# Performance work log

Measured on AMD Instinct MI355X. Metric: run time of the kernel, lower is better.

## Reference

```python
import jax, jax.numpy as jnp
import numpy as np

DIM = 256
HEADS = 8
WS = 8      # window size
SS = 4      # shift size
EPS = 1e-5
HEAD_DIM = DIM // HEADS
SCALE = HEAD_DIM ** (-0.5)
N = WS * WS

# relative position index, replicating tf.meshgrid default 'xy' indexing
_ch = np.arange(WS)
_coords = np.stack(np.meshgrid(_ch, _ch, indexing='xy'))          # [2, WS, WS]
_flat = _coords.reshape(2, -1)                                     # [2, N]
_rel = _flat[:, :, None] - _flat[:, None, :]                       # [2, N, N]
_rel = _rel.transpose(1, 2, 0) + np.array([WS - 1, WS - 1])
_rel = _rel * np.array([2 * WS - 1, 1])
RPI = jnp.asarray(_rel.sum(-1).reshape(-1))                        # [N*N] int


def _calc_mask(H, W):
    # faithful to source: mask is -100 where window region ids are EQUAL, 0 otherwise
    img = np.zeros((H, W))
    slices = (slice(0, -WS), slice(-WS, -SS), slice(-SS, None))
    cnt = 0
    for hs in slices:
        for ws_ in slices:
            img[hs, ws_] = cnt
            cnt += 1
    mw = img.reshape(H // WS, WS, W // WS, WS).transpose(0, 2, 1, 3).reshape(-1, N)
    diff = mw[:, None, :] - mw[:, :, None]
    mask = np.where(diff == 0, -100.0, 0.0).astype(np.float32)     # [nW, N, N]
    return jnp.asarray(mask)


def _layernorm(x, g, b):
    m = jnp.mean(x, axis=-1, keepdims=True)
    v = jnp.mean(jnp.square(x - m), axis=-1, keepdims=True)
    return (x - m) * jax.lax.rsqrt(v + EPS) * g + b


def setup_inputs() -> dict:
    key = jax.random.key(0)
    ks = jax.random.split(key, 8)
    B, L, C = 16, 64 * 64, DIM
    s = 0.02
    return {
        'x': jax.random.normal(ks[0], (B, L, C), jnp.float32),
        'norm1_g': jnp.ones((C,), jnp.float32),
        'norm1_b': jnp.zeros((C,), jnp.float32),
        'qkv_w': jax.random.normal(ks[1], (C, 3 * C), jnp.float32) * s,
        'qkv_b': jnp.zeros((3 * C,), jnp.float32),
        'rpb_table': jax.random.normal(ks[2], ((2 * WS - 1) ** 2, HEADS), jnp.float32) * s,
        'proj_w': jax.random.normal(ks[3], (C, C), jnp.float32) * s,
        'proj_b': jnp.zeros((C,), jnp.float32),
        'norm2_g': jnp.ones((C,), jnp.float32),
        'norm2_b': jnp.zeros((C,), jnp.float32),
        'fc1_w': jax.random.normal(ks[4], (C, 4 * C), jnp.float32) * s,
        'fc1_b': jnp.zeros((4 * C,), jnp.float32),
        'fc2_w': jax.random.normal(ks[5], (4 * C, C), jnp.float32) * s,
        'fc2_b': jnp.zeros((C,), jnp.float32),
        'h': 64,
        'w': 64,
    }


def reference(x, norm1_g, norm1_b, qkv_w, qkv_b, rpb_table, proj_w, proj_b,
              norm2_g, norm2_b, fc1_w, fc1_b, fc2_w, fc2_b, h, w):
    B, L, C = x.shape
    nH, nW = h // WS, w // WS
    nWin = nH * nW
    shortcut = x

    xn = _layernorm(x, norm1_g, norm1_b).reshape(B, h, w, C)
    xn = jnp.roll(xn, shift=(-SS, -SS), axis=(1, 2))                 # cyclic shift
    # window partition -> [B*nWin, N, C]
    xw = xn.reshape(B, nH, WS, nW, WS, C).transpose(0, 1, 3, 2, 4, 5).reshape(B * nWin, N, C)

    qkv = (xw @ qkv_w + qkv_b).reshape(B * nWin, N, 3, HEADS, HEAD_DIM)
    qkv = qkv.transpose(2, 0, 3, 1, 4)                               # [3, B*nWin, H, N, d]
    q, k, v = qkv[0] * SCALE, qkv[1], qkv[2]

    attn = jnp.einsum('bhnd,bhmd->bhnm', q, k)                       # [B*nWin, H, N, N]
    bias = rpb_table[RPI].reshape(N, N, HEADS).transpose(2, 0, 1)    # [H, N, N]
    attn = attn + bias[None]

    mask = _calc_mask(h, w)                                          # [nWin, N, N]
    attn = attn.reshape(B, nWin, HEADS, N, N) + mask[None, :, None]
    attn = jax.nn.softmax(attn, axis=-1).reshape(B * nWin, HEADS, N, N)

    out = jnp.einsum('bhnm,bhmd->bhnd', attn, v)                     # [B*nWin, H, N, d]
    out = out.transpose(0, 2, 1, 3).reshape(B * nWin, N, C)
    out = out @ proj_w + proj_b

    # window reverse + reverse shift
    out = out.reshape(B, nH, nW, WS, WS, C).transpose(0, 1, 3, 2, 4, 5).reshape(B, h, w, C)
    out = jnp.roll(out, shift=(SS, SS), axis=(1, 2)).reshape(B, h * w, C)

    y = shortcut + out
    m = _layernorm(y, norm2_g, norm2_b)
    m = jax.nn.gelu(m @ fc1_w + fc1_b, approximate=False) @ fc2_w + fc2_b
    # faithful to source: final residual reuses the ORIGINAL shortcut, not y
    return shortcut + m
```

## Files before the change

kernel.cpp:

```cpp
#include <hip/hip_runtime.h>
#include <math.h>

typedef __bf16 bf16;
typedef __bf16 bf16x4 __attribute__((ext_vector_type(4)));
typedef __bf16 bf16x8 __attribute__((ext_vector_type(8)));
typedef float f32x4 __attribute__((ext_vector_type(4)));

#define AS1 __attribute__((address_space(1)))
#define AS3 __attribute__((address_space(3)))

__device__ __forceinline__ void gload_lds16(const bf16* g, bf16* l) {
    __builtin_amdgcn_global_load_lds((const AS1 void*)g, (AS3 void*)l, 16, 0, 0);
}

__device__ __forceinline__ float gelu_fast(float v) {
    const float u = 1.5957691216057308f * (v + 0.044715f * v * v * v);
    return v / (1.0f + __expf(-u));
}

__global__ __launch_bounds__(256)
void wprep_all(const float* __restrict__ qkv_w, const float* __restrict__ proj_w,
               const float* __restrict__ fc1_w, const float* __restrict__ fc2_w,
               bf16* __restrict__ qkv_wt, bf16* __restrict__ proj_wt,
               bf16* __restrict__ fc1_wt, bf16* __restrict__ fc2_wt)
{
    int idx = blockIdx.x * 256 + threadIdx.x;
    const float* src; bf16* dst; int K, N;
    if (idx < 196608)            { src = qkv_w;  dst = qkv_wt;  K = 256;  N = 768; }
    else if (idx < 262144)       { idx -= 196608; src = proj_w; dst = proj_wt; K = 256;  N = 256; }
    else if (idx < 524288)       { idx -= 262144; src = fc1_w;  dst = fc1_wt;  K = 256;  N = 1024; }
    else                         { idx -= 524288; src = fc2_w;  dst = fc2_wt;  K = 1024; N = 256; }
    const int k = idx / N, n = idx % N;
    dst[(long)n * K + k] = (bf16)src[idx];
}

__global__ __launch_bounds__(256)
void ln1_window(const float* __restrict__ x, const float* __restrict__ g,
                const float* __restrict__ be, bf16* __restrict__ xw)
{
    const int t = threadIdx.x;
    const int lane = t & 63;
    const int w = t >> 6;
    const long tok = (long)blockIdx.x * 4 + w;
    const float4 v = ((const float4*)(x + tok * 256))[lane];
    float sum = v.x + v.y + v.z + v.w;
    float sq  = v.x * v.x + v.y * v.y + v.z * v.z + v.w * v.w;
#pragma unroll
    for (int m = 32; m >= 1; m >>= 1) {
        sum += __shfl_xor(sum, m, 64);
        sq  += __shfl_xor(sq,  m, 64);
    }
    const float mean = sum * (1.0f / 256.0f);
    const float var  = sq * (1.0f / 256.0f) - mean * mean;
    const float rstd = rsqrtf(var + 1e-5f);
    const float4 gv = ((const float4*)g)[lane];
    const float4 bv = ((const float4*)be)[lane];
    bf16x4 ov;
    ov[0] = (bf16)((v.x - mean) * rstd * gv.x + bv.x);
    ov[1] = (bf16)((v.y - mean) * rstd * gv.y + bv.y);
    ov[2] = (bf16)((v.z - mean) * rstd * gv.z + bv.z);
    ov[3] = (bf16)((v.w - mean) * rstd * gv.w + bv.w);
    const int b = (int)(tok >> 12);
    const int l = (int)(tok & 4095);
    const int i = l >> 6, j = l & 63;
    const int ip = (i + 60) & 63, jp = (j + 60) & 63;
    const int winl = ((ip >> 3) << 3) + (jp >> 3);
    const int n = ((ip & 7) << 3) + (jp & 7);
    const long drow = ((long)b * 64 + winl) * 64 + n;
    *(bf16x4*)(xw + drow * 256 + lane * 4) = ov;
}

__global__ __launch_bounds__(256)
void ln2_kernel(const float* __restrict__ x, const bf16* __restrict__ pj,
                const float* __restrict__ g, const float* __restrict__ be,
                bf16* __restrict__ xn2)
{
    const int t = threadIdx.x;
    const int lane = t & 63;
    const int w = t >> 6;
    const long tok = (long)blockIdx.x * 4 + w;
    const float4 xv = ((const float4*)(x + tok * 256))[lane];
    const bf16x4 pv = *(const bf16x4*)(pj + tok * 256 + lane * 4);
    float y0 = xv.x + (float)pv[0];
    float y1 = xv.y + (float)pv[1];
    float y2 = xv.z + (float)pv[2];
    float y3 = xv.w + (float)pv[3];
    float sum = y0 + y1 + y2 + y3;
    float sq  = y0 * y0 + y1 * y1 + y2 * y2 + y3 * y3;
#pragma unroll
    for (int m = 32; m >= 1; m >>= 1) {
        sum += __shfl_xor(sum, m, 64);
        sq  += __shfl_xor(sq,  m, 64);
    }
    const float mean = sum * (1.0f / 256.0f);
    const float var  = sq * (1.0f / 256.0f) - mean * mean;
    const float rstd = rsqrtf(var + 1e-5f);
    const float4 gv = ((const float4*)g)[lane];
    const float4 bv = ((const float4*)be)[lane];
    bf16x4 ov;
    ov[0] = (bf16)((y0 - mean) * rstd * gv.x + bv.x);
    ov[1] = (bf16)((y1 - mean) * rstd * gv.y + bv.y);
    ov[2] = (bf16)((y2 - mean) * rstd * gv.z + bv.z);
    ov[3] = (bf16)((y3 - mean) * rstd * gv.w + bv.w);
    *(bf16x4*)(xn2 + tok * 256 + lane * 4) = ov;
}

template<int EPI>
__global__ __launch_bounds__(512, 2)
void gemm_w(const bf16* __restrict__ A, const bf16* __restrict__ Bt,
            const float* __restrict__ bias, void* __restrict__ outp,
            int N, int K, const float* __restrict__ xres, int gx, int nb)
{
    extern __shared__ bf16 lds[];
    bf16* sA = lds;
    bf16* sB = lds + 3 * 8192;
    const int t = threadIdx.x;
    const int l = t & 63;
    const int w = t >> 6;
    const int wr = w >> 1, wc = w & 1;
    const int q = nb >> 3;
    const int id = ((int)blockIdx.x & 7) * q + ((int)blockIdx.x >> 3);
    const long m0 = (long)(id / gx) * 256;
    const long n0 = (long)(id % gx) * 128;

    long asrc[2]; int adst[2];
#pragma unroll
    for (int j = 0; j < 2; j++) {
        const int idx = j * 512 + t;
        const int p = idx >> 3, s = idx & 7;
        const int sl = s ^ (p & 7);
        const int row = 2 * p + (sl >> 2);
        const int ce = (sl & 3) * 8;
        asrc[j] = (m0 + row) * (long)K + ce;
        adst[j] = idx * 8;
    }
    long bsrc; int bdst;
    {
        const int idx = t;
        const int p = idx >> 3, s = idx & 7;
        const int sl = s ^ (p & 7);
        const int row = 2 * p + (sl >> 2);
        const int ce = (sl & 3) * 8;
        bsrc = (n0 + row) * (long)K + ce;
        bdst = idx * 8;
    }

    f32x4 acc[4][4];
#pragma unroll
    for (int i = 0; i < 4; i++)
#pragma unroll
        for (int j = 0; j < 4; j++) acc[i][j] = (f32x4){0.f, 0.f, 0.f, 0.f};

    const int KT = K >> 5;
    const int c = l >> 4;
    const int ra = wr * 64 + (l & 15);
    const int rb = wc * 64 + (l & 15);

#define STAGE(bufi, ko)                                                        \
    do {                                                                       \
        gload_lds16(A + asrc[0] + (ko), &sA[(bufi) * 8192 + adst[0]]);         \
        gload_lds16(A + asrc[1] + (ko), &sA[(bufi) * 8192 + adst[1]]);         \
        gload_lds16(Bt + bsrc + (ko), &sB[(bufi) * 4096 + bdst]);              \
    } while (0)

#define COMPUTE(bufi)                                                          \
    do {                                                                       \
        bf16x8 av[4], bv[4];                                                   \
        _Pragma("unroll")                                                      \
        for (int ni = 0; ni < 4; ni++) {                                       \
            const int row = rb + ni * 16;                                      \
            const int p = row >> 1;                                            \
            const int s = (((row & 1) << 2) + c) ^ (p & 7);                    \
            bv[ni] = *(const bf16x8*)&sB[(bufi) * 4096 + (p * 8 + s) * 8];     \
        }                                                                      \
        _Pragma("unroll")                                                      \
        for (int mi = 0; mi < 4; mi++) {                                       \
            const int row = ra + mi * 16;                                      \
            const int p = row >> 1;                                            \
            const int s = (((row & 1) << 2) + c) ^ (p & 7);                    \
            av[mi] = *(const bf16x8*)&sA[(bufi) * 8192 + (p * 8 + s) * 8];     \
        }                                                                      \
        _Pragma("unroll")                                                      \
        for (int mi = 0; mi < 4; mi++)                                         \
            _Pragma("unroll")                                                  \
            for (int ni = 0; ni < 4; ni++)                                     \
                acc[mi][ni] = __builtin_amdgcn_mfma_f32_16x16x32_bf16(         \
                    bv[ni], av[mi], acc[mi][ni], 0, 0, 0);                     \
    } while (0)

    STAGE(0, 0);
    STAGE(1, 32);

    int buf = 0;
    for (int kt = 0; kt < KT - 1; ++kt) {
        asm volatile("s_waitcnt vmcnt(3)" ::: "memory");
        __builtin_amdgcn_s_barrier();
        __builtin_amdgcn_sched_barrier(0);
        if (kt + 2 < KT) {
            const int nbuf = (buf + 2 >= 3) ? buf - 1 : buf + 2;
            STAGE(nbuf, (long)(kt + 2) * 32);
        }
        COMPUTE(buf);
        buf = (buf + 1 == 3) ? 0 : buf + 1;
    }
    asm volatile("s_waitcnt vmcnt(0)" ::: "memory");
    __builtin_amdgcn_s_barrier();
    __builtin_amdgcn_sched_barrier(0);
    COMPUTE(buf);
#undef STAGE
#undef COMPUTE

#pragma unroll
    for (int mi = 0; mi < 4; mi++)
#pragma unroll
        for (int ni = 0; ni < 4; ni++) {
            const long row = m0 + wr * 64 + mi * 16 + (l & 15);
            const int col = (int)(n0 + wc * 64 + ni * 16 + (l >> 4) * 4);
            const float4 bz = *(const float4*)&bias[col];
            float v0 = acc[mi][ni][0] + bz.x;
            float v1 = acc[mi][ni][1] + bz.y;
            float v2 = acc[mi][ni][2] + bz.z;
            float v3 = acc[mi][ni][3] + bz.w;
            if constexpr (EPI == 2) {
                v0 = gelu_fast(v0); v1 = gelu_fast(v1);
                v2 = gelu_fast(v2); v3 = gelu_fast(v3);
            }
            if constexpr (EPI == 3) {
                const float4 xr = *(const float4*)&xres[row * N + col];
                float4 ov = {v0 + xr.x, v1 + xr.y, v2 + xr.z, v3 + xr.w};
                *(float4*)&((float*)outp)[row * N + col] = ov;
            } else {
                bf16x4 ov;
                ov[0] = (bf16)v0; ov[1] = (bf16)v1; ov[2] = (bf16)v2; ov[3] = (bf16)v3;
                if constexpr (EPI == 1) {
                    const int gwin = (int)(row >> 6);
                    const int n = (int)(row & 63);
                    const int bb = gwin >> 6, wi = gwin & 63;
                    const int ipp = ((wi >> 3) << 3) + (n >> 3);
                    const int jpp = ((wi & 7) << 3) + (n & 7);
                    const int ii = (ipp + 4) & 63, jj = (jpp + 4) & 63;
                    const long tok = ((long)bb << 12) + (ii << 6) + jj;
                    *(bf16x4*)&((bf16*)outp)[tok * 256 + col] = ov;
                } else {
                    *(bf16x4*)&((bf16*)outp)[row * N + col] = ov;
                }
            }
        }
    (void)xres;
}

__global__ __launch_bounds__(256, 2)
void attn_kernel(const bf16* __restrict__ qkv, const float* __restrict__ rpb,
                 bf16* __restrict__ out)
{
    __shared__ bf16 P_lds[4][64 * 64];
    const int t = threadIdx.x;
    const int lane = t & 63;
    const int w = t >> 6;
    const int win = blockIdx.x;
    const int wi = win & 63;
    const int lr = lane & 15;
    const int lg = lane >> 4;
    const int lk = lg * 8;
    const long base = (long)win * 64 * 768;
    const float scale = 0.17677669529663687f;
    const int whb = (wi >> 3) << 3;
    const int wwb = (wi & 7) << 3;
    const f32x4 z4 = {0.f, 0.f, 0.f, 0.f};

    for (int hh = 0; hh < 2; hh++) {
        const int head = w + hh * 4;
        const bf16* qp = qkv + base + head * 32;
        const bf16* kp = qkv + base + 256 + head * 32;
        const bf16* vp = qkv + base + 512 + head * 32;

        bf16x8 aq[4], bk[4];
#pragma unroll
        for (int mi = 0; mi < 4; mi++)
            aq[mi] = *(const bf16x8*)(qp + (mi * 16 + lr) * 768 + lk);
#pragma unroll
        for (int ni = 0; ni < 4; ni++)
            bk[ni] = *(const bf16x8*)(kp + (ni * 16 + lr) * 768 + lk);

        f32x4 s[4][4];
#pragma unroll
        for (int i = 0; i < 4; i++)
#pragma unroll
            for (int j = 0; j < 4; j++) s[i][j] = z4;
#pragma unroll
        for (int mi = 0; mi < 4; mi++)
#pragma unroll
            for (int ni = 0; ni < 4; ni++)
                s[mi][ni] = __builtin_amdgcn_mfma_f32_16x16x32_bf16(aq[mi], bk[ni], s[mi][ni], 0, 0, 0);

#pragma unroll
        for (int mi = 0; mi < 4; mi++)
#pragma unroll
            for (int r = 0; r < 4; r++) {
                const int n = mi * 16 + lg * 4 + r;
                const int gi = whb + (n >> 3);
                const int gj = wwb + (n & 7);
                const int idn = (gi < 56 ? 0 : (gi < 60 ? 1 : 2)) * 3 + (gj < 56 ? 0 : (gj < 60 ? 1 : 2));
                float vals[4];
                float rowmax = -3.0e38f;
#pragma unroll
                for (int ni = 0; ni < 4; ni++) {
                    const int m = ni * 16 + lr;
                    const int gi2 = whb + (m >> 3);
                    const int gj2 = wwb + (m & 7);
                    const int idm = (gi2 < 56 ? 0 : (gi2 < 60 ? 1 : 2)) * 3 + (gj2 < 56 ? 0 : (gj2 < 60 ? 1 : 2));
                    const int dj = (n & 7) - (m & 7);
                    const int di = (n >> 3) - (m >> 3);
                    float sv = s[mi][ni][r] * scale + rpb[((dj + 7) * 15 + (di + 7)) * 8 + head];
                    if (idn == idm) sv -= 100.0f;
                    vals[ni] = sv;
                    rowmax = fmaxf(rowmax, sv);
                }
#pragma unroll
                for (int msk = 8; msk >= 1; msk >>= 1)
                    rowmax = fmaxf(rowmax, __shfl_xor(rowmax, msk, 64));
                float rsum = 0.f;
#pragma unroll
                for (int ni = 0; ni < 4; ni++) {
                    const float p = __expf(vals[ni] - rowmax);
                    vals[ni] = p;
                    rsum += p;
                }
#pragma unroll
                for (int msk = 8; msk >= 1; msk >>= 1)
                    rsum += __shfl_xor(rsum, msk, 64);
                const float inv = 1.0f / rsum;
#pragma unroll
                for (int ni = 0; ni < 4; ni++)
                    P_lds[w][n * 64 + ni * 16 + lr] = (bf16)(vals[ni] * inv);
            }

        f32x4 o[4][2];
#pragma unroll
        for (int i = 0; i < 4; i++)
#pragma unroll
            for (int j = 0; j < 2; j++) o[i][j] = z4;
#pragma unroll
        for (int kk = 0; kk < 2; kk++) {
            bf16x8 bv[2];
#pragma unroll
            for (int ni = 0; ni < 2; ni++)
#pragma unroll
                for (int i = 0; i < 8; i++)
                    bv[ni][i] = vp[(kk * 32 + lk + i) * 768 + ni * 16 + lr];
#pragma unroll
            for (int mi = 0; mi < 4; mi++) {
                const bf16x8 ap = *(const bf16x8*)&P_lds[w][(mi * 16 + lr) * 64 + kk * 32 + lk];
#pragma unroll
                for (int ni = 0; ni < 2; ni++)
                    o[mi][ni] = __builtin_amdgcn_mfma_f32_16x16x32_bf16(bv[ni], ap, o[mi][ni], 0, 0, 0);
            }
        }
#pragma unroll
        for (int mi = 0; mi < 4; mi++)
#pragma unroll
            for (int ni = 0; ni < 2; ni++) {
                const int n = mi * 16 + lr;
                const int d = ni * 16 + lg * 4;
                bf16x4 ov;
                ov[0] = (bf16)o[mi][ni][0]; ov[1] = (bf16)o[mi][ni][1];
                ov[2] = (bf16)o[mi][ni][2]; ov[3] = (bf16)o[mi][ni][3];
                *(bf16x4*)(out + ((long)(win * 64 + n)) * 256 + head * 32 + d) = ov;
            }
    }
}

extern "C" void kernel_launch(void* const* d_in, const int* in_sizes, int n_in,
                              void* d_out, int out_size, void* d_ws, size_t ws_size,
                              hipStream_t stream)
{
    (void)in_sizes; (void)n_in; (void)out_size;
    const float* x      = (const float*)d_in[0];
    const float* n1g    = (const float*)d_in[1];
    const float* n1b    = (const float*)d_in[2];
    const float* qkv_w  = (const float*)d_in[3];
    const float* qkv_b  = (const float*)d_in[4];
    const float* rpb    = (const float*)d_in[5];
    const float* proj_w = (const float*)d_in[6];
    const float* proj_b = (const float*)d_in[7];
    const float* n2g    = (const float*)d_in[8];
    const float* n2b    = (const float*)d_in[9];
    const float* fc1_w  = (const float*)d_in[10];
    const float* fc1_b  = (const float*)d_in[11];
    const float* fc2_w  = (const float*)d_in[12];
    const float* fc2_b  = (const float*)d_in[13];
    float* out = (float*)d_out;

    char* ws = (char*)d_ws;
    bf16* qkv_wt  = (bf16*)(ws + 0);
    bf16* proj_wt = (bf16*)(ws + 393216);
    bf16* fc1_wt  = (bf16*)(ws + 524288);
    bf16* fc2_wt  = (bf16*)(ws + 1048576);
    bf16* xw      = (bf16*)(ws + 2097152);
    bf16* qkvb    = (bf16*)(ws + 35651584);
    bf16* attn_o  = xw;
    bf16* proj_o  = qkvb;
    bf16* xn2     = (bf16*)d_out;
    bf16* hbuf    = xw;
    if (ws_size < 136314880ull) return;

    const size_t LB = 73728;

    wprep_all<<<3072, 256, 0, stream>>>(qkv_w, proj_w, fc1_w, fc2_w,
                                        qkv_wt, proj_wt, fc1_wt, fc2_wt);

    ln1_window<<<16384, 256, 0, stream>>>(x, n1g, n1b, xw);
    gemm_w<0><<<1536, 512, LB, stream>>>(xw, qkv_wt, qkv_b, qkvb, 768, 256, nullptr, 6, 1536);
    attn_kernel<<<1024, 256, 0, stream>>>(qkvb, rpb, attn_o);
    gemm_w<1><<<512, 512, LB, stream>>>(attn_o, proj_wt, proj_b, proj_o, 256, 256, nullptr, 2, 512);
    ln2_kernel<<<16384, 256, 0, stream>>>(x, proj_o, n2g, n2b, xn2);
    gemm_w<2><<<2048, 512, LB, stream>>>(xn2, fc1_wt, fc1_b, hbuf, 1024, 256, nullptr, 8, 2048);
    gemm_w<3><<<512, 512, LB, stream>>>(hbuf, fc2_wt, fc2_b, out, 256, 1024, x, 2, 512);
}
```

Measured before the change: 321.1 us.

## Write V transposed per window from QKV GEMM and split attention heads across blocks

The QKV GEMM epilogue now writes the V third of its output in a per-window transposed layout into a scratch buffer (the output buffer, reused before LN2). The attention kernel can then load V with vector 16-byte reads instead of strided scalar gathers. Attention is also split into two blocks per window, one head per wave, with a higher occupancy bound. The P tile in LDS is XOR-swizzled to cut bank conflicts. The risk is that the transposed V stores in the GEMM epilogue are scattered 2-byte writes, which may slow the QKV GEMM.

```diff
diff --git a/kernel.cpp b/kernel.cpp
--- a/kernel.cpp
+++ b/kernel.cpp
@@ -109,7 +109,8 @@
 __global__ __launch_bounds__(512, 2)
 void gemm_w(const bf16* __restrict__ A, const bf16* __restrict__ Bt,
             const float* __restrict__ bias, void* __restrict__ outp,
-            int N, int K, const float* __restrict__ xres, int gx, int nb)
+            int N, int K, const float* __restrict__ xres, void* __restrict__ aux,
+            int gx, int nb)
 {
     extern __shared__ bf16 lds[];
     bf16* sA = lds;
@@ -217,21 +218,37 @@
             const long row = m0 + wr * 64 + mi * 16 + (l & 15);
             const int col = (int)(n0 + wc * 64 + ni * 16 + (l >> 4) * 4);
             const float4 bz = *(const float4*)&bias[col];
-            float v0 = acc[mi][ni][0] + bz.x;
-            float v1 = acc[mi][ni][1] + bz.y;
-            float v2 = acc[mi][ni][2] + bz.z;
-            float v3 = acc[mi][ni][3] + bz.w;
+            float vv[4];
+            vv[0] = acc[mi][ni][0] + bz.x;
+            vv[1] = acc[mi][ni][1] + bz.y;
+            vv[2] = acc[mi][ni][2] + bz.z;
+            vv[3] = acc[mi][ni][3] + bz.w;
             if constexpr (EPI == 2) {
-                v0 = gelu_fast(v0); v1 = gelu_fast(v1);
-                v2 = gelu_fast(v2); v3 = gelu_fast(v3);
+#pragma unroll
+                for (int j = 0; j < 4; j++) vv[j] = gelu_fast(vv[j]);
             }
             if constexpr (EPI == 3) {
                 const float4 xr = *(const float4*)&xres[row * N + col];
-                float4 ov = {v0 + xr.x, v1 + xr.y, v2 + xr.z, v3 + xr.w};
+                float4 ov = {vv[0] + xr.x, vv[1] + xr.y, vv[2] + xr.z, vv[3] + xr.w};
                 *(float4*)&((float*)outp)[row * N + col] = ov;
+            } else if constexpr (EPI == 0) {
+                if (col >= 512) {
+                    bf16* vt = (bf16*)aux;
+                    const int win = (int)(row >> 6);
+                    const int n = (int)(row & 63);
+#pragma unroll
+                    for (int j = 0; j < 4; j++)
+                        vt[(long)win * 16384 + (col - 512 + j) * 64 + n] = (bf16)vv[j];
+                } else {
+                    bf16x4 ov;
+#pragma unroll
+                    for (int j = 0; j < 4; j++) ov[j] = (bf16)vv[j];
+                    *(bf16x4*)&((bf16*)outp)[row * N + col] = ov;
+                }
             } else {
                 bf16x4 ov;
-                ov[0] = (bf16)v0; ov[1] = (bf16)v1; ov[2] = (bf16)v2; ov[3] = (bf16)v3;
+#pragma unroll
+                for (int j = 0; j < 4; j++) ov[j] = (bf16)vv[j];
                 if constexpr (EPI == 1) {
                     const int gwin = (int)(row >> 6);
                     const int n = (int)(row & 63);
@@ -246,18 +263,19 @@
                 }
             }
         }
-    (void)xres;
-}
-
-__global__ __launch_bounds__(256, 2)
-void attn_kernel(const bf16* __restrict__ qkv, const float* __restrict__ rpb,
-                 bf16* __restrict__ out)
+    (void)xres; (void)aux;
+}
+
+__global__ __launch_bounds__(256, 4)
+void attn_kernel(const bf16* __restrict__ qkv, const bf16* __restrict__ vT,
+                 const float* __restrict__ rpb, bf16* __restrict__ out)
 {
     __shared__ bf16 P_lds[4][64 * 64];
     const int t = threadIdx.x;
     const int lane = t & 63;
     const int w = t >> 6;
-    const int win = blockIdx.x;
+    const int win = blockIdx.x >> 1;
+    const int head = (blockIdx.x & 1) * 4 + w;
     const int wi = win & 63;
     const int lr = lane & 15;
     const int lg = lane >> 4;
@@ -268,106 +286,108 @@
     const int wwb = (wi & 7) << 3;
     const f32x4 z4 = {0.f, 0.f, 0.f, 0.f};
 
-    for (int hh = 0; hh < 2; hh++) {
-        const int head = w + hh * 4;
-        const bf16* qp = qkv + base + head * 32;
-        const bf16* kp = qkv + base + 256 + head * 32;
-        const bf16* vp = qkv + base + 512 + head * 32;
-
-        bf16x8 aq[4], bk[4];
-#pragma unroll
-        for (int mi = 0; mi < 4; mi++)
-            aq[mi] = *(const bf16x8*)(qp + (mi * 16 + lr) * 768 + lk);
+    const bf16* qp  = qkv + base + head * 32;
+    const bf16* kp  = qkv + base + 256 + head * 32;
+    const bf16* vtp = vT + (long)win * 16384 + head * 32 * 64;
+
+    int idm[4];
+#pragma unroll
+    for (int ni = 0; ni < 4; ni++) {
+        const int m = ni * 16 + lr;
+        const int gi2 = whb + (m >> 3), gj2 = wwb + (m & 7);
+        idm[ni] = (gi2 < 56 ? 0 : (gi2 < 60 ? 1 : 2)) * 3 + (gj2 < 56 ? 0 : (gj2 < 60 ? 1 : 2));
+    }
+
+    bf16x8 aq[4], bk[4];
+#pragma unroll
+    for (int mi = 0; mi < 4; mi++)
+        aq[mi] = *(const bf16x8*)(qp + (mi * 16 + lr) * 768 + lk);
+#pragma unroll
+    for (int ni = 0; ni < 4; ni++)
+        bk[ni] = *(const bf16x8*)(kp + (ni * 16 + lr) * 768 + lk);
+
+    f32x4 s[4][4];
+#pragma unroll
+    for (int i = 0; i < 4; i++)
+#pragma unroll
+        for (int j = 0; j < 4; j++) s[i][j] = z4;
+#pragma unroll
+    for (int mi = 0; mi < 4; mi++)
 #pragma unroll
         for (int ni = 0; ni < 4; ni++)
-            bk[ni] = *(const bf16x8*)(kp + (ni * 16 + lr) * 768 + lk);
-
-        f32x4 s[4][4];
-#pragma unroll
-        for (int i = 0; i < 4; i++)
-#pragma unroll
-            for (int j = 0; j < 4; j++) s[i][j] = z4;
-#pragma unroll
-        for (int mi = 0; mi < 4; mi++)
+            s[mi][ni] = __builtin_amdgcn_mfma_f32_16x16x32_bf16(aq[mi], bk[ni], s[mi][ni], 0, 0, 0);
+
+#pragma unroll
+    for (int mi = 0; mi < 4; mi++)
+#pragma unroll
+        for (int r = 0; r < 4; r++) {
+            const int n = mi * 16 + lg * 4 + r;
+            const int gi = whb + (n >> 3);
+            const int gj = wwb + (n & 7);
+            const int idn = (gi < 56 ? 0 : (gi < 60 ? 1 : 2)) * 3 + (gj < 56 ? 0 : (gj < 60 ? 1 : 2));
+            float vals[4];
+            float rowmax = -3.0e38f;
+#pragma unroll
+            for (int ni = 0; ni < 4; ni++) {
+                const int m = ni * 16 + lr;
+                const int dj = (n & 7) - (m & 7);
+                const int di = (n >> 3) - (m >> 3);
+                float sv = s[mi][ni][r] * scale + rpb[((dj + 7) * 15 + (di + 7)) * 8 + head];
+                if (idn == idm[ni]) sv -= 100.0f;
+                vals[ni] = sv;
+                rowmax = fmaxf(rowmax, sv);
+            }
+#pragma unroll
+            for (int msk = 8; msk >= 1; msk >>= 1)
+                rowmax = fmaxf(rowmax, __shfl_xor(rowmax, msk, 64));
+            float rsum = 0.f;
+#pragma unroll
+            for (int ni = 0; ni < 4; ni++) {
+                const float p = __expf(vals[ni] - rowmax);
+                vals[ni] = p;
+                rsum += p;
+            }
+#pragma unroll
+            for (int msk = 8; msk >= 1; msk >>= 1)
+                rsum += __shfl_xor(rsum, msk, 64);
+            const float inv = 1.0f / rsum;
+            const int swz = (n & 7) << 3;
 #pragma unroll
             for (int ni = 0; ni < 4; ni++)
-                s[mi][ni] = __builtin_amdgcn_mfma_f32_16x16x32_bf16(aq[mi], bk[ni], s[mi][ni], 0, 0, 0);
-
-#pragma unroll
-        for (int mi = 0; mi < 4; mi++)
-#pragma unroll
-            for (int r = 0; r < 4; r++) {
-                const int n = mi * 16 + lg * 4 + r;
-                const int gi = whb + (n >> 3);
-                const int gj = wwb + (n & 7);
-                const int idn = (gi < 56 ? 0 : (gi < 60 ? 1 : 2)) * 3 + (gj < 56 ? 0 : (gj < 60 ? 1 : 2));
-                float vals[4];
-                float rowmax = -3.0e38f;
-#pragma unroll
-                for (int ni = 0; ni < 4; ni++) {
-                    const int m = ni * 16 + lr;
-                    const int gi2 = whb + (m >> 3);
-                    const int gj2 = wwb + (m & 7);
-                    const int idm = (gi2 < 56 ? 0 : (gi2 < 60 ? 1 : 2)) * 3 + (gj2 < 56 ? 0 : (gj2 < 60 ? 1 : 2));
-                    const int dj = (n & 7) - (m & 7);
-                    const int di = (n >> 3) - (m >> 3);
-                    float sv = s[mi][ni][r] * scale + rpb[((dj + 7) * 15 + (di + 7)) * 8 + head];
-                    if (idn == idm) sv -= 100.0f;
-                    vals[ni] = sv;
-                    rowmax = fmaxf(rowmax, sv);
-                }
-#pragma unroll
-                for (int msk = 8; msk >= 1; msk >>= 1)
-                    rowmax = fmaxf(rowmax, __shfl_xor(rowmax, msk, 64));
-                float rsum = 0.f;
-#pragma unroll
-                for (int ni = 0; ni < 4; ni++) {
-                    const float p = __expf(vals[ni] - rowmax);
-                    vals[ni] = p;
-                    rsum += p;
-                }
-#pragma unroll
-                for (int msk = 8; msk >= 1; msk >>= 1)
-                    rsum += __shfl_xor(rsum, msk, 64);
-                const float inv = 1.0f / rsum;
-#pragma unroll
-                for (int ni = 0; ni < 4; ni++)
-                    P_lds[w][n * 64 + ni * 16 + lr] = (bf16)(vals[ni] * inv);
-            }
-
-        f32x4 o[4][2];
-#pragma unroll
-        for (int i = 0; i < 4; i++)
-#pragma unroll
-            for (int j = 0; j < 2; j++) o[i][j] = z4;
-#pragma unroll
-        for (int kk = 0; kk < 2; kk++) {
-            bf16x8 bv[2];
+                P_lds[w][n * 64 + ((ni * 16 + lr) ^ swz)] = (bf16)(vals[ni] * inv);
+        }
+
+    f32x4 o[4][2];
+#pragma unroll
+    for (int i = 0; i < 4; i++)
+#pragma unroll
+        for (int j = 0; j < 2; j++) o[i][j] = z4;
+#pragma unroll
+    for (int kk = 0; kk < 2; kk++) {
+        bf16x8 bv[2];
+#pragma unroll
+        for (int ni = 0; ni < 2; ni++)
+            bv[ni] = *(const bf16x8*)&vtp[(ni * 16 + lr) * 64 + kk * 32 + lk];
+#pragma unroll
+        for (int mi = 0; mi < 4; mi++) {
+            const int row = mi * 16 + lr;
+            const bf16x8 ap = *(const bf16x8*)&P_lds[w][row * 64 + ((kk * 32 + lk) ^ ((row & 7) << 3))];
 #pragma unroll
             for (int ni = 0; ni < 2; ni++)
-#pragma unroll
-                for (int i = 0; i < 8; i++)
-                    bv[ni][i] = vp[(kk * 32 + lk + i) * 768 + ni * 16 + lr];
-#pragma unroll
-            for (int mi = 0; mi < 4; mi++) {
-                const bf16x8 ap = *(const bf16x8*)&P_lds[w][(mi * 16 + lr) * 64 + kk * 32 + lk];
-#pragma unroll
-                for (int ni = 0; ni < 2; ni++)
-                    o[mi][ni] = __builtin_amdgcn_mfma_f32_16x16x32_bf16(bv[ni], ap, o[mi][ni], 0, 0, 0);
-            }
+                o[mi][ni] = __builtin_amdgcn_mfma_f32_16x16x32_bf16(bv[ni], ap, o[mi][ni], 0, 0, 0);
         }
-#pragma unroll
-        for (int mi = 0; mi < 4; mi++)
-#pragma unroll
-            for (int ni = 0; ni < 2; ni++) {
-                const int n = mi * 16 + lr;
-                const int d = ni * 16 + lg * 4;
-                bf16x4 ov;
-                ov[0] = (bf16)o[mi][ni][0]; ov[1] = (bf16)o[mi][ni][1];
-                ov[2] = (bf16)o[mi][ni][2]; ov[3] = (bf16)o[mi][ni][3];
-                *(bf16x4*)(out + ((long)(win * 64 + n)) * 256 + head * 32 + d) = ov;
-            }
-    }
+    }
+#pragma unroll
+    for (int mi = 0; mi < 4; mi++)
+#pragma unroll
+        for (int ni = 0; ni < 2; ni++) {
+            const int n = mi * 16 + lr;
+            const int d = ni * 16 + lg * 4;
+            bf16x4 ov;
+            ov[0] = (bf16)o[mi][ni][0]; ov[1] = (bf16)o[mi][ni][1];
+            ov[2] = (bf16)o[mi][ni][2]; ov[3] = (bf16)o[mi][ni][3];
+            *(bf16x4*)(out + ((long)(win * 64 + n)) * 256 + head * 32 + d) = ov;
+        }
 }
 
 extern "C" void kernel_launch(void* const* d_in, const int* in_sizes, int n_in,
@@ -400,6 +420,7 @@
     bf16* qkvb    = (bf16*)(ws + 35651584);
     bf16* attn_o  = xw;
     bf16* proj_o  = qkvb;
+    bf16* vT      = (bf16*)d_out;
     bf16* xn2     = (bf16*)d_out;
     bf16* hbuf    = xw;
     if (ws_size < 136314880ull) return;
@@ -410,10 +431,10 @@
                                         qkv_wt, proj_wt, fc1_wt, fc2_wt);
 
     ln1_window<<<16384, 256, 0, stream>>>(x, n1g, n1b, xw);
-    gemm_w<0><<<1536, 512, LB, stream>>>(xw, qkv_wt, qkv_b, qkvb, 768, 256, nullptr, 6, 1536);
-    attn_kernel<<<1024, 256, 0, stream>>>(qkvb, rpb, attn_o);
-    gemm_w<1><<<512, 512, LB, stream>>>(attn_o, proj_wt, proj_b, proj_o, 256, 256, nullptr, 2, 512);
+    gemm_w<0><<<1536, 512, LB, stream>>>(xw, qkv_wt, qkv_b, qkvb, 768, 256, nullptr, vT, 6, 1536);
+    attn_kernel<<<2048, 256, 0, stream>>>(qkvb, vT, rpb, attn_o);
+    gemm_w<1><<<512, 512, LB, stream>>>(attn_o, proj_wt, proj_b, proj_o, 256, 256, nullptr, nullptr, 2, 512);
     ln2_kernel<<<16384, 256, 0, stream>>>(x, proj_o, n2g, n2b, xn2);
-    gemm_w<2><<<2048, 512, LB, stream>>>(xn2, fc1_wt, fc1_b, hbuf, 1024, 256, nullptr, 8, 2048);
-    gemm_w<3><<<512, 512, LB, stream>>>(hbuf, fc2_wt, fc2_b, out, 256, 1024, x, 2, 512);
-}
+    gemm_w<2><<<2048, 512, LB, stream>>>(xn2, fc1_wt, fc1_b, hbuf, 1024, 256, nullptr, nullptr, 8, 2048);
+    gemm_w<3><<<512, 512, LB, stream>>>(hbuf, fc2_wt, fc2_b, out, 256, 1024, x, nullptr, 2, 512);
+}
```

Result: faster. 290.4 us (-9.6%).
